# Kernel tuning notes

Measured on AMD Instinct MI355X. Metric: run time of the kernel, lower is better.

Reference implementation:

```python
import jax, jax.numpy as jnp
import numpy as np

N, E, IN_DIM, H, D = 50000, 1600000, 128, 8, 16


def setup_inputs() -> dict:
    key = jax.random.key(0)
    ks = jax.random.split(key, 9)
    s = 1.0 / np.sqrt(IN_DIM)
    return {
        "h": jax.random.normal(ks[0], (N, IN_DIM), dtype=jnp.float32),
        "Wq": jax.random.normal(ks[1], (IN_DIM, H * D), dtype=jnp.float32) * s,
        "bq": jax.random.normal(ks[2], (H * D,), dtype=jnp.float32) * 0.01,
        "Wk": jax.random.normal(ks[3], (IN_DIM, H * D), dtype=jnp.float32) * s,
        "bk": jax.random.normal(ks[4], (H * D,), dtype=jnp.float32) * 0.01,
        "Wv": jax.random.normal(ks[5], (IN_DIM, H * D), dtype=jnp.float32) * s,
        "bv": jax.random.normal(ks[6], (H * D,), dtype=jnp.float32) * 0.01,
        "src": jax.random.randint(ks[7], (E,), 0, N, dtype=jnp.int32),
        "dst": jax.random.randint(ks[8], (E,), 0, N, dtype=jnp.int32),
    }


def reference(h, Wq, bq, Wk, bk, Wv, bv, src, dst):
    n = h.shape[0]
    # node-level projections, reshaped to [N, H, D]
    Q = (h @ Wq + bq).reshape(n, H, D)
    K = (h @ Wk + bk).reshape(n, H, D)
    V = (h @ Wv + bv).reshape(n, H, D)
    # per-edge score: dot(K[src], Q[dst]) / sqrt(D), exp-clamped -> [E, H]
    score = jnp.sum(K[src] * Q[dst], axis=-1) / np.sqrt(D)
    score = jnp.exp(jnp.clip(score, -5.0, 5.0))
    # score-weighted messages scattered into destination nodes
    m = V[src] * score[:, :, None]                    # [E, H, D]
    wV = jax.ops.segment_sum(m, dst, num_segments=n)  # [N, H, D]
    z = jax.ops.segment_sum(score, dst, num_segments=n)  # [N, H]
    h_out = wV / (z[:, :, None] + 1e-6)
    return h_out.reshape(n, H * D)
```

## Files before the change

kernel.cpp:

```cpp
#include <hip/hip_runtime.h>
#include <hip/hip_bf16.h>

#define IN_DIM 128
#define HH 8
#define DD 16
#define HD 128
#define SCAN_B 256
#define CHUNK 8192

#define MT  64
#define KP  136
#define NCH 128

#define VPAD 132

typedef float f32x4 __attribute__((ext_vector_type(4)));
typedef short s16x8 __attribute__((ext_vector_type(8)));

__device__ __forceinline__ int sniff_fp32(const unsigned short* h_raw) {
  int sane = 0;
#pragma unroll
  for (int i = 0; i < 128; i += 2) {
    const unsigned short u = h_raw[i];
    const int expo = (u >> 7) & 0xFF;
    if (expo >= 112 && expo <= 143) sane++;
  }
  return (sane >= 40) ? 0 : 1;
}

__global__ __launch_bounds__(128) void wt_kernel(
    const unsigned short* __restrict__ h_raw,
    const void* __restrict__ Wq, const void* __restrict__ Wk,
    const void* __restrict__ Wv, __hip_bfloat16* __restrict__ Wt,
    int* __restrict__ flag, int* __restrict__ bucket_size) {
  const int isf = sniff_fp32(h_raw);
  const int n = blockIdx.x;
  const int k = threadIdx.x;
  if (n == 0) {
    if (k == 0) *flag = isf;
    for (int j = k; j < 258; j += 128) bucket_size[j] = 0;
  }
  const int mat = n >> 7;
  const int col = n & 127;
  const void* W = (mat == 0) ? Wq : (mat == 1) ? Wk : Wv;
  float v;
  if (isf) v = ((const float*)W)[(size_t)k * HD + col];
  else     v = __bfloat162float(((const __hip_bfloat16*)W)[(size_t)k * HD + col]);
  Wt[(size_t)n * KP + k] = __float2bfloat16(v);
}

__global__ __launch_bounds__(256) void proj_hist_kernel(
    const void* __restrict__ h, const __hip_bfloat16* __restrict__ Wt,
    const void* __restrict__ bq, const void* __restrict__ bk,
    const void* __restrict__ bv,
    float* __restrict__ Qf, __hip_bfloat16* __restrict__ Kb,
    __hip_bfloat16* __restrict__ Vb,
    const int* __restrict__ flag, int n_nodes,
    const int* __restrict__ dst, int* __restrict__ bucket_size, int n_edges,
    int pgrid) {
  __shared__ short Bs[NCH * KP];
  __shared__ short As[MT * KP];

  const int tid = threadIdx.x;

  if (blockIdx.x >= pgrid) {
    int* lh = (int*)Bs;
    const int e0 = (blockIdx.x - pgrid) * CHUNK;
    const int e1 = (e0 + CHUNK < n_edges) ? e0 + CHUNK : n_edges;
    lh[tid] = 0;
    __syncthreads();
    for (int e = e0 + tid; e < e1; e += 256) atomicAdd(&lh[dst[e] >> 8], 1);
    __syncthreads();
    if (lh[tid] > 0) atomicAdd(&bucket_size[tid], lh[tid]);
    return;
  }

  const int node0 = blockIdx.x * MT;
  const int isf = *flag;

#pragma unroll
  for (int j = 0; j < 16; ++j) {
    const int pid = tid + j * 256;
    const int m = pid >> 6;
    const int kk = (pid & 63) * 2;
    const int g = node0 + m;
    unsigned int pack = 0;
    if (g < n_nodes) {
      if (isf) {
        const float2 f2 = *(const float2*)((const float*)h + (size_t)g * HD + kk);
        const __hip_bfloat16 b0 = __float2bfloat16(f2.x);
        const __hip_bfloat16 b1 = __float2bfloat16(f2.y);
        pack = (unsigned int)(*(const unsigned short*)&b0) |
               ((unsigned int)(*(const unsigned short*)&b1) << 16);
      } else {
        pack = *(const unsigned int*)((const __hip_bfloat16*)h +
                                      (size_t)g * HD + kk);
      }
    }
    *(unsigned int*)&As[m * KP + kk] = pack;
  }
  __syncthreads();

  const int wave = tid >> 6;
  const int lane = tid & 63;
  const int l15 = lane & 15;
  const int quad = lane >> 4;

  s16x8 afrag[4];
#pragma unroll
  for (int k4 = 0; k4 < 4; ++k4)
    afrag[k4] = *(const s16x8*)&As[(wave * 16 + l15) * KP + k4 * 32 + quad * 8];

  for (int c = 0; c < 3; ++c) {
    __syncthreads();
    const uint4* gsrc = (const uint4*)(Wt + (size_t)c * NCH * KP);
    for (int j = tid; j < (NCH * KP * 2) / 16; j += 256)
      ((uint4*)Bs)[j] = gsrc[j];
    __syncthreads();

    f32x4 acc[8];
#pragma unroll
    for (int t = 0; t < 8; ++t) acc[t] = (f32x4){0.f, 0.f, 0.f, 0.f};

#pragma unroll
    for (int t = 0; t < 8; ++t) {
#pragma unroll
      for (int k4 = 0; k4 < 4; ++k4) {
        const s16x8 bfrag =
            *(const s16x8*)&Bs[(t * 16 + l15) * KP + k4 * 32 + quad * 8];
        acc[t] = __builtin_amdgcn_mfma_f32_16x16x32_bf16(afrag[k4], bfrag,
                                                         acc[t], 0, 0, 0);
      }
    }

    const void* bp = (c == 0) ? bq : (c == 1) ? bk : bv;
#pragma unroll
    for (int t = 0; t < 8; ++t) {
      const int ncol = t * 16 + l15;
      const float bias = isf ? ((const float*)bp)[ncol]
                             : __bfloat162float(((const __hip_bfloat16*)bp)[ncol]);
#pragma unroll
      for (int r = 0; r < 4; ++r) {
        const int g = node0 + wave * 16 + quad * 4 + r;
        if (g < n_nodes) {
          const float val = acc[t][r] + bias;
          const size_t o = (size_t)g * HD + ncol;
          if (c == 0)      Qf[o] = val;
          else if (c == 1) Kb[o] = __float2bfloat16(val);
          else             Vb[o] = __float2bfloat16(val);
        }
      }
    }
  }
}

__global__ __launch_bounds__(256) void bucket_scan_kernel(
    const int* __restrict__ bucket_size, int* __restrict__ bucket_base,
    int* __restrict__ bucket_cur, int nbuck, int n_edges) {
  __shared__ int sh[256];
  const int t = threadIdx.x;
  const int v = (t < nbuck) ? bucket_size[t] : 0;
  sh[t] = v;
  __syncthreads();
  for (int off = 1; off < 256; off <<= 1) {
    int add = (t >= off) ? sh[t - off] : 0;
    __syncthreads();
    sh[t] += add;
    __syncthreads();
  }
  const int excl = sh[t] - v;
  if (t < nbuck) {
    bucket_base[t] = excl;
    bucket_cur[t] = excl;
  }
  if (t == 0) bucket_base[nbuck] = n_edges;
}

__global__ __launch_bounds__(256) void bucketize_kernel(
    const int* __restrict__ src, const int* __restrict__ dst,
    int* __restrict__ bucket_cur, unsigned int* __restrict__ ebuf,
    int n_edges) {
  __shared__ int lh[256];
  const int t = threadIdx.x;
  const int e0 = blockIdx.x * CHUNK;
  const int e1 = (e0 + CHUNK < n_edges) ? e0 + CHUNK : n_edges;
  lh[t] = 0;
  __syncthreads();
  for (int e = e0 + t; e < e1; e += 256) atomicAdd(&lh[dst[e] >> 8], 1);
  __syncthreads();
  const int cnt_local = lh[t];
  int base = 0;
  if (cnt_local > 0) base = atomicAdd(&bucket_cur[t], cnt_local);
  __syncthreads();
  lh[t] = base;
  __syncthreads();
  for (int e = e0 + t; e < e1; e += 256) {
    const int d = dst[e];
    const int pos = atomicAdd(&lh[d >> 8], 1);
    ebuf[pos] = ((unsigned int)src[e] << 16) | (unsigned int)d;
  }
}

__global__ __launch_bounds__(256) void bucket_csr_kernel(
    const unsigned int* __restrict__ ebuf, const int* __restrict__ bucket_base,
    int* __restrict__ row_ptr, int* __restrict__ edge_src,
    int n_nodes, int nbuck) {
  __shared__ int lc[256];
  __shared__ int sh[256];
  const int b = blockIdx.x;
  const int t = threadIdx.x;
  const int lo = bucket_base[b], hi = bucket_base[b + 1];
  const int nbase = b << 8;

  lc[t] = 0;
  __syncthreads();
  for (int i = lo + t; i < hi; i += 256)
    atomicAdd(&lc[(ebuf[i] & 0xFFFFu) - nbase], 1);
  __syncthreads();

  const int v = lc[t];
  sh[t] = v;
  __syncthreads();
  for (int off = 1; off < 256; off <<= 1) {
    int add = (t >= off) ? sh[t - off] : 0;
    __syncthreads();
    sh[t] += add;
    __syncthreads();
  }
  const int excl = sh[t] - v;

  const int node = nbase + t;
  if (node < n_nodes) row_ptr[node] = lo + excl;
  if (b == nbuck - 1 && t == 255) row_ptr[n_nodes] = hi;

  __syncthreads();
  lc[t] = lo + excl;
  __syncthreads();
  for (int i = lo + t; i < hi; i += 256) {
    const unsigned int pkd = ebuf[i];
    const int pos = atomicAdd(&lc[(pkd & 0xFFFFu) - nbase], 1);
    edge_src[pos] = (int)(pkd >> 16);
  }
}

__global__ __launch_bounds__(256) void hist_kernel(
    const int* __restrict__ dst, int* __restrict__ cnt, int n_edges) {
  const int e = blockIdx.x * blockDim.x + threadIdx.x;
  if (e < n_edges) atomicAdd(&cnt[dst[e]], 1);
}

__global__ __launch_bounds__(256) void scatter_kernel(
    const int* __restrict__ src, const int* __restrict__ dst,
    int* __restrict__ cursor, int* __restrict__ edge_src, int n_edges) {
  const int e = blockIdx.x * blockDim.x + threadIdx.x;
  if (e < n_edges) {
    const int pos = atomicAdd(&cursor[dst[e]], 1);
    edge_src[pos] = src[e];
  }
}

__global__ __launch_bounds__(SCAN_B) void scan1_kernel(
    const int* __restrict__ cnt, int* __restrict__ exs,
    int* __restrict__ bsum, int n) {
  __shared__ int sh[SCAN_B];
  const int t = threadIdx.x;
  const int i = blockIdx.x * SCAN_B + t;
  int v = (i < n) ? cnt[i] : 0;
  sh[t] = v;
  __syncthreads();
  for (int off = 1; off < SCAN_B; off <<= 1) {
    int add = (t >= off) ? sh[t - off] : 0;
    __syncthreads();
    sh[t] += add;
    __syncthreads();
  }
  if (i < n) exs[i] = sh[t] - v;
  if (t == SCAN_B - 1) bsum[blockIdx.x] = sh[t];
}

__global__ __launch_bounds__(SCAN_B) void scan2_kernel(int* __restrict__ bsum,
                                                       int nb) {
  __shared__ int sh[SCAN_B];
  const int t = threadIdx.x;
  if (nb <= SCAN_B) {
    int v = (t < nb) ? bsum[t] : 0;
    sh[t] = v;
    __syncthreads();
    for (int off = 1; off < SCAN_B; off <<= 1) {
      int add = (t >= off) ? sh[t - off] : 0;
      __syncthreads();
      sh[t] += add;
      __syncthreads();
    }
    if (t < nb) bsum[t] = sh[t] - v;
  } else if (t == 0) {
    int run = 0;
    for (int b = 0; b < nb; ++b) { int v = bsum[b]; bsum[b] = run; run += v; }
  }
}

__global__ __launch_bounds__(SCAN_B) void scan3_kernel(
    const int* __restrict__ exs, const int* __restrict__ bsum,
    int* __restrict__ row_ptr, int* __restrict__ cursor, int n, int n_edges) {
  const int i = blockIdx.x * SCAN_B + threadIdx.x;
  if (i < n) {
    const int v = exs[i] + bsum[blockIdx.x];
    row_ptr[i] = v;
    cursor[i] = v;
  }
  if (i == 0) row_ptr[n] = n_edges;
}

__global__ __launch_bounds__(128) void gather_kernel(
    const int* __restrict__ row_ptr, const int* __restrict__ edge_src,
    const float* __restrict__ Qf, const __hip_bfloat16* __restrict__ Kb,
    const __hip_bfloat16* __restrict__ Vb,
    void* __restrict__ out, const int* __restrict__ flag, int n_nodes) {
  __shared__ float vred[16][VPAD];
  __shared__ float zred[16][HH];

  const int d = blockIdx.x;
  const int tid = threadIdx.x;

  const int eloc = tid >> 3;
  const int hh8  = tid & 7;

  const int start = row_ptr[d];
  const int deg = row_ptr[d + 1] - start;

  float qreg[16];
  {
    const f32x4* qp = (const f32x4*)(Qf + (size_t)d * HD + hh8 * 16);
#pragma unroll
    for (int j = 0; j < 4; ++j) {
      const f32x4 q4 = qp[j];
      qreg[j * 4 + 0] = q4[0] * 0.25f;
      qreg[j * 4 + 1] = q4[1] * 0.25f;
      qreg[j * 4 + 2] = q4[2] * 0.25f;
      qreg[j * 4 + 3] = q4[3] * 0.25f;
    }
  }

  float acc[16];
#pragma unroll
  for (int j = 0; j < 16; ++j) acc[j] = 0.0f;
  float zacc = 0.0f;

  int s_next = 0;
  if (eloc < deg) s_next = edge_src[start + eloc];

  for (int ei = eloc; ei < deg; ei += 16) {
    const int s = s_next;
    const int nx = ei + 16;
    if (nx < deg) s_next = edge_src[start + nx];

    const size_t rowoff = (size_t)s * HD + hh8 * 16;
    const uint4* kp = (const uint4*)(Kb + rowoff);
    const uint4 k0 = kp[0];
    const uint4 k1 = kp[1];
    const uint4* vp = (const uint4*)(Vb + rowoff);
    const uint4 v0 = vp[0];
    const uint4 v1 = vp[1];

    unsigned int kw[8];
    *(uint4*)&kw[0] = k0;
    *(uint4*)&kw[4] = k1;
    float dot = 0.0f;
#pragma unroll
    for (int i = 0; i < 8; ++i) {
      const float klo = __uint_as_float(kw[i] << 16);
      const float khi = __uint_as_float(kw[i] & 0xFFFF0000u);
      dot = fmaf(qreg[2 * i], klo, dot);
      dot = fmaf(qreg[2 * i + 1], khi, dot);
    }
    const float score = __expf(fminf(fmaxf(dot, -5.0f), 5.0f));
    zacc += score;

    unsigned int vw[8];
    *(uint4*)&vw[0] = v0;
    *(uint4*)&vw[4] = v1;
#pragma unroll
    for (int i = 0; i < 8; ++i) {
      const float vlo = __uint_as_float(vw[i] << 16);
      const float vhi = __uint_as_float(vw[i] & 0xFFFF0000u);
      acc[2 * i]     = fmaf(score, vlo, acc[2 * i]);
      acc[2 * i + 1] = fmaf(score, vhi, acc[2 * i + 1]);
    }
  }

#pragma unroll
  for (int j = 0; j < 16; ++j) vred[eloc][hh8 * 16 + j] = acc[j];
  zred[eloc][hh8] = zacc;
  __syncthreads();

  const int hd16 = tid >> 4;
  float sumV = 0.0f;
#pragma unroll
  for (int i = 0; i < 16; ++i) sumV += vred[i][tid];
  float sumZ = 0.0f;
#pragma unroll
  for (int i = 0; i < 16; ++i) sumZ += zred[i][hd16];

  const float r = sumV / (sumZ + 1e-6f);
  const size_t o = (size_t)d * HD + tid;
  if (*flag) ((float*)out)[o] = r;
  else       ((__hip_bfloat16*)out)[o] = __float2bfloat16(r);
}

extern "C" void kernel_launch(void* const* d_in, const int* in_sizes, int n_in,
                              void* d_out, int out_size, void* d_ws, size_t ws_size,
                              hipStream_t stream) {
  const void* h  = d_in[0];
  const void* Wq = d_in[1];
  const void* bq = d_in[2];
  const void* Wk = d_in[3];
  const void* bk = d_in[4];
  const void* Wv = d_in[5];
  const void* bv = d_in[6];
  const int* src = (const int*)d_in[7];
  const int* dst = (const int*)d_in[8];

  const int n_nodes = in_sizes[0] / IN_DIM;
  const int n_edges = in_sizes[7];
  const int nb = (n_nodes + SCAN_B - 1) / SCAN_B;
  const int nbuck = (n_nodes + 255) >> 8;

  char* p = (char*)d_ws;
  int* flag = (int*)p;                       p += 256;
  float* Qf = (float*)p;                     p += (size_t)n_nodes * HD * 4;
  __hip_bfloat16* Kb = (__hip_bfloat16*)p;   p += (size_t)n_nodes * HD * 2;
  __hip_bfloat16* Vb = (__hip_bfloat16*)p;   p += (size_t)n_nodes * HD * 2;
  __hip_bfloat16* Wt = (__hip_bfloat16*)p;   p += ((size_t)384 * KP * 2 + 255) / 256 * 256;
  int* bucket_size = (int*)p;                p += 258 * 4;
  int* bucket_base = (int*)p;                p += 258 * 4;
  int* bucket_cur = (int*)p;                 p += 258 * 4;
  int* row_ptr = (int*)p;                    p += (size_t)(n_nodes + 1) * 4;
  unsigned int* ebuf = (unsigned int*)p;     p += (size_t)n_edges * 4;
  int* edge_src = (int*)p;                   p += (size_t)n_edges * 4;
  int* cnt = (int*)p;                        p += (size_t)n_nodes * 4;
  int* exs = (int*)p;                        p += (size_t)n_nodes * 4;
  int* bsum = (int*)p;                       p += (size_t)(nb + 1) * 4;
  int* cursor = (int*)p;                     p += (size_t)n_nodes * 4;

  wt_kernel<<<384, 128, 0, stream>>>((const unsigned short*)h, Wq, Wk, Wv, Wt,
                                     flag, bucket_size);

  const int pgrid = (n_nodes + MT - 1) / MT;
  const int nchunk = (n_edges + CHUNK - 1) / CHUNK;

  if (n_nodes <= 65536) {
    proj_hist_kernel<<<pgrid + nchunk, 256, 0, stream>>>(
        h, Wt, bq, bk, bv, Qf, Kb, Vb, flag, n_nodes, dst, bucket_size,
        n_edges, pgrid);
    bucket_scan_kernel<<<1, 256, 0, stream>>>(bucket_size, bucket_base,
                                              bucket_cur, nbuck, n_edges);
    bucketize_kernel<<<nchunk, 256, 0, stream>>>(src, dst, bucket_cur, ebuf,
                                                 n_edges);
    bucket_csr_kernel<<<nbuck, 256, 0, stream>>>(ebuf, bucket_base, row_ptr,
                                                 edge_src, n_nodes, nbuck);
  } else {
    proj_hist_kernel<<<pgrid, 256, 0, stream>>>(
        h, Wt, bq, bk, bv, Qf, Kb, Vb, flag, n_nodes, dst, bucket_size,
        n_edges, pgrid);
    hipMemsetAsync(cnt, 0, (size_t)n_nodes * sizeof(int), stream);
    const int eb = 256;
    const int egrid = (n_edges + eb - 1) / eb;
    hist_kernel<<<egrid, eb, 0, stream>>>(dst, cnt, n_edges);
    scan1_kernel<<<nb, SCAN_B, 0, stream>>>(cnt, exs, bsum, n_nodes);
    scan2_kernel<<<1, SCAN_B, 0, stream>>>(bsum, nb);
    scan3_kernel<<<nb, SCAN_B, 0, stream>>>(exs, bsum, row_ptr, cursor,
                                            n_nodes, n_edges);
    scatter_kernel<<<egrid, eb, 0, stream>>>(src, dst, cursor, edge_src,
                                             n_edges);
  }

  gather_kernel<<<n_nodes, 128, 0, stream>>>(row_ptr, edge_src, Qf, Kb, Vb,
                                             d_out, flag, n_nodes);
}
```

Measured before the change: 320.8 us.

## Interleave K and V per node and process two edges per iteration in gather

```diff
diff --git a/kernel.cpp b/kernel.cpp
--- a/kernel.cpp
+++ b/kernel.cpp
@@ -11,8 +11,6 @@
 #define MT  64
 #define KP  136
 #define NCH 128
-
-#define VPAD 132
 
 typedef float f32x4 __attribute__((ext_vector_type(4)));
 typedef short s16x8 __attribute__((ext_vector_type(8)));
@@ -53,8 +51,7 @@
     const void* __restrict__ h, const __hip_bfloat16* __restrict__ Wt,
     const void* __restrict__ bq, const void* __restrict__ bk,
     const void* __restrict__ bv,
-    float* __restrict__ Qf, __hip_bfloat16* __restrict__ Kb,
-    __hip_bfloat16* __restrict__ Vb,
+    float* __restrict__ Qf, __hip_bfloat16* __restrict__ KVb,
     const int* __restrict__ flag, int n_nodes,
     const int* __restrict__ dst, int* __restrict__ bucket_size, int n_edges,
     int pgrid) {
@@ -144,10 +141,13 @@
         const int g = node0 + wave * 16 + quad * 4 + r;
         if (g < n_nodes) {
           const float val = acc[t][r] + bias;
-          const size_t o = (size_t)g * HD + ncol;
-          if (c == 0)      Qf[o] = val;
-          else if (c == 1) Kb[o] = __float2bfloat16(val);
-          else             Vb[o] = __float2bfloat16(val);
+          if (c == 0) {
+            Qf[(size_t)g * HD + ncol] = val;
+          } else if (c == 1) {
+            KVb[(size_t)g * 256 + ncol] = __float2bfloat16(val);
+          } else {
+            KVb[(size_t)g * 256 + 128 + ncol] = __float2bfloat16(val);
+          }
         }
       }
     }
@@ -313,10 +313,9 @@
 
 __global__ __launch_bounds__(128) void gather_kernel(
     const int* __restrict__ row_ptr, const int* __restrict__ edge_src,
-    const float* __restrict__ Qf, const __hip_bfloat16* __restrict__ Kb,
-    const __hip_bfloat16* __restrict__ Vb,
+    const float* __restrict__ Qf, const __hip_bfloat16* __restrict__ KVb,
     void* __restrict__ out, const int* __restrict__ flag, int n_nodes) {
-  __shared__ float vred[16][VPAD];
+  __shared__ float vred[HD][17];
   __shared__ float zred[16][HH];
 
   const int d = blockIdx.x;
@@ -346,57 +345,79 @@
   for (int j = 0; j < 16; ++j) acc[j] = 0.0f;
   float zacc = 0.0f;
 
-  int s_next = 0;
-  if (eloc < deg) s_next = edge_src[start + eloc];
-
-  for (int ei = eloc; ei < deg; ei += 16) {
-    const int s = s_next;
-    const int nx = ei + 16;
-    if (nx < deg) s_next = edge_src[start + nx];
-
-    const size_t rowoff = (size_t)s * HD + hh8 * 16;
-    const uint4* kp = (const uint4*)(Kb + rowoff);
-    const uint4 k0 = kp[0];
-    const uint4 k1 = kp[1];
-    const uint4* vp = (const uint4*)(Vb + rowoff);
-    const uint4 v0 = vp[0];
-    const uint4 v1 = vp[1];
+  int s0 = 0, s1 = 0;
+  if (eloc < deg) s0 = edge_src[start + eloc];
+  if (eloc + 16 < deg) s1 = edge_src[start + eloc + 16];
+
+  for (int ei = eloc; ei < deg; ei += 32) {
+    const int sA = s0;
+    const bool hasB = (ei + 16 < deg);
+    const int sB = hasB ? s1 : sA;
+
+    const int nx = ei + 32;
+    if (nx < deg) s0 = edge_src[start + nx];
+    if (nx + 16 < deg) s1 = edge_src[start + nx + 16];
+
+    const uint4* pA = (const uint4*)(KVb + (size_t)sA * 256 + hh8 * 16);
+    const uint4* pB = (const uint4*)(KVb + (size_t)sB * 256 + hh8 * 16);
+    const uint4 kA0 = pA[0], kA1 = pA[1];
+    const uint4 vA0 = pA[16], vA1 = pA[17];
+    const uint4 kB0 = pB[0], kB1 = pB[1];
+    const uint4 vB0 = pB[16], vB1 = pB[17];
 
     unsigned int kw[8];
-    *(uint4*)&kw[0] = k0;
-    *(uint4*)&kw[4] = k1;
-    float dot = 0.0f;
+    *(uint4*)&kw[0] = kA0;
+    *(uint4*)&kw[4] = kA1;
+    float dotA = 0.0f;
 #pragma unroll
     for (int i = 0; i < 8; ++i) {
       const float klo = __uint_as_float(kw[i] << 16);
       const float khi = __uint_as_float(kw[i] & 0xFFFF0000u);
-      dot = fmaf(qreg[2 * i], klo, dot);
-      dot = fmaf(qreg[2 * i + 1], khi, dot);
-    }
-    const float score = __expf(fminf(fmaxf(dot, -5.0f), 5.0f));
-    zacc += score;
-
-    unsigned int vw[8];
-    *(uint4*)&vw[0] = v0;
-    *(uint4*)&vw[4] = v1;
+      dotA = fmaf(qreg[2 * i], klo, dotA);
+      dotA = fmaf(qreg[2 * i + 1], khi, dotA);
+    }
+    *(uint4*)&kw[0] = kB0;
+    *(uint4*)&kw[4] = kB1;
+    float dotB = 0.0f;
 #pragma unroll
     for (int i = 0; i < 8; ++i) {
-      const float vlo = __uint_as_float(vw[i] << 16);
-      const float vhi = __uint_as_float(vw[i] & 0xFFFF0000u);
-      acc[2 * i]     = fmaf(score, vlo, acc[2 * i]);
-      acc[2 * i + 1] = fmaf(score, vhi, acc[2 * i + 1]);
-    }
-  }
-
-#pragma unroll
-  for (int j = 0; j < 16; ++j) vred[eloc][hh8 * 16 + j] = acc[j];
+      const float klo = __uint_as_float(kw[i] << 16);
+      const float khi = __uint_as_float(kw[i] & 0xFFFF0000u);
+      dotB = fmaf(qreg[2 * i], klo, dotB);
+      dotB = fmaf(qreg[2 * i + 1], khi, dotB);
+    }
+    const float scoreA = __expf(fminf(fmaxf(dotA, -5.0f), 5.0f));
+    float scoreB = __expf(fminf(fmaxf(dotB, -5.0f), 5.0f));
+    if (!hasB) scoreB = 0.0f;
+    zacc += scoreA + scoreB;
+
+    unsigned int vwA[8], vwB[8];
+    *(uint4*)&vwA[0] = vA0;
+    *(uint4*)&vwA[4] = vA1;
+    *(uint4*)&vwB[0] = vB0;
+    *(uint4*)&vwB[4] = vB1;
+#pragma unroll
+    for (int i = 0; i < 8; ++i) {
+      const float vAlo = __uint_as_float(vwA[i] << 16);
+      const float vAhi = __uint_as_float(vwA[i] & 0xFFFF0000u);
+      const float vBlo = __uint_as_float(vwB[i] << 16);
+      const float vBhi = __uint_as_float(vwB[i] & 0xFFFF0000u);
+      acc[2 * i]     = fmaf(scoreA, vAlo, acc[2 * i]);
+      acc[2 * i]     = fmaf(scoreB, vBlo, acc[2 * i]);
+      acc[2 * i + 1] = fmaf(scoreA, vAhi, acc[2 * i + 1]);
+      acc[2 * i + 1] = fmaf(scoreB, vBhi, acc[2 * i + 1]);
+    }
+  }
+
+#pragma unroll
+  for (int j = 0; j < 16; ++j) vred[hh8 * 16 + j][eloc] = acc[j];
   zred[eloc][hh8] = zacc;
   __syncthreads();
 
   const int hd16 = tid >> 4;
   float sumV = 0.0f;
 #pragma unroll
-  for (int i = 0; i < 16; ++i) sumV += vred[i][tid];
+  for (int i = 0; i < 16; ++i) sumV += vred[tid][i];
   float sumZ = 0.0f;
 #pragma unroll
   for (int i = 0; i < 16; ++i) sumZ += zred[i][hd16];
@@ -428,8 +449,7 @@
   char* p = (char*)d_ws;
   int* flag = (int*)p;                       p += 256;
   float* Qf = (float*)p;                     p += (size_t)n_nodes * HD * 4;
-  __hip_bfloat16* Kb = (__hip_bfloat16*)p;   p += (size_t)n_nodes * HD * 2;
-  __hip_bfloat16* Vb = (__hip_bfloat16*)p;   p += (size_t)n_nodes * HD * 2;
+  __hip_bfloat16* KVb = (__hip_bfloat16*)p;  p += (size_t)n_nodes * 256 * 2;
   __hip_bfloat16* Wt = (__hip_bfloat16*)p;   p += ((size_t)384 * KP * 2 + 255) / 256 * 256;
   int* bucket_size = (int*)p;                p += 258 * 4;
   int* bucket_base = (int*)p;                p += 258 * 4;
@@ -450,7 +470,7 @@
 
   if (n_nodes <= 65536) {
     proj_hist_kernel<<<pgrid + nchunk, 256, 0, stream>>>(
-        h, Wt, bq, bk, bv, Qf, Kb, Vb, flag, n_nodes, dst, bucket_size,
+        h, Wt, bq, bk, bv, Qf, KVb, flag, n_nodes, dst, bucket_size,
         n_edges, pgrid);
     bucket_scan_kernel<<<1, 256, 0, stream>>>(bucket_size, bucket_base,
                                               bucket_cur, nbuck, n_edges);
@@ -460,7 +480,7 @@
                                                  edge_src, n_nodes, nbuck);
   } else {
     proj_hist_kernel<<<pgrid, 256, 0, stream>>>(
-        h, Wt, bq, bk, bv, Qf, Kb, Vb, flag, n_nodes, dst, bucket_size,
+        h, Wt, bq, bk, bv, Qf, KVb, flag, n_nodes, dst, bucket_size,
         n_edges, pgrid);
     hipMemsetAsync(cnt, 0, (size_t)n_nodes * sizeof(int), stream);
     const int eb = 256;
@@ -474,6 +494,6 @@
                                              n_edges);
   }
 
-  gather_kernel<<<n_nodes, 128, 0, stream>>>(row_ptr, edge_src, Qf, Kb, Vb,
+  gather_kernel<<<n_nodes, 128, 0, stream>>>(row_ptr, edge_src, Qf, KVb,
                                              d_out, flag, n_nodes);
 }
```

Result: no change. 317.4 us (-1.1%).
